# Kernel tuning notes

Measured on AMD Instinct MI355X. Metric: run time of the kernel, lower is better.

The kernel has to match this reference:

```python
import jax, jax.numpy as jnp
import numpy as np

D_MODEL = 1024
D_FF = 4096
NUM_EXPERTS = 8
TOP_K = 2


def setup_inputs() -> dict:
    key = jax.random.key(0)
    ks = jax.random.split(key, 9)
    s_in = 1.0 / np.sqrt(D_MODEL)
    s_ff = 1.0 / np.sqrt(D_FF)
    return {
        "x": jax.random.normal(ks[0], (2, 1024, D_MODEL), dtype=jnp.float32),
        "Wg": jax.random.uniform(ks[1], (D_MODEL, NUM_EXPERTS), minval=-s_in, maxval=s_in, dtype=jnp.float32),
        "bg": jax.random.uniform(ks[2], (NUM_EXPERTS,), minval=-s_in, maxval=s_in, dtype=jnp.float32),
        "W1": jax.random.uniform(ks[3], (NUM_EXPERTS, D_MODEL, D_FF), minval=-s_in, maxval=s_in, dtype=jnp.float32),
        "b1": jax.random.uniform(ks[4], (NUM_EXPERTS, D_FF), minval=-s_in, maxval=s_in, dtype=jnp.float32),
        "W2": jax.random.uniform(ks[5], (NUM_EXPERTS, D_MODEL, D_FF), minval=-s_in, maxval=s_in, dtype=jnp.float32),
        "b2": jax.random.uniform(ks[6], (NUM_EXPERTS, D_FF), minval=-s_in, maxval=s_in, dtype=jnp.float32),
        "W3": jax.random.uniform(ks[7], (NUM_EXPERTS, D_FF, D_MODEL), minval=-s_ff, maxval=s_ff, dtype=jnp.float32),
        "b3": jax.random.uniform(ks[8], (NUM_EXPERTS, D_MODEL), minval=-s_ff, maxval=s_ff, dtype=jnp.float32),
    }


def reference(x, Wg, bg, W1, b1, W2, b2, W3, b3):
    B, S, D = x.shape
    xf = x.reshape(-1, D)                                   # [N, D]
    N = xf.shape[0]

    # ---- Router (eval mode: no noise) ----
    logits = xf @ Wg + bg                                   # [N, E]
    top_logits, top_idx = jax.lax.top_k(logits, TOP_K)      # [N, K]
    top_w = jax.nn.softmax(top_logits, axis=-1)             # softmax over the top-k logits
    # scatter top-k weights into dense [N, E]; indices are unique per row
    comb_w = jnp.zeros_like(logits).at[jnp.arange(N)[:, None], top_idx].set(top_w)

    # ---- Experts: GLU-MLP, dense per-expert (weights are 0 for unrouted tokens) ----
    h1 = jnp.einsum('nd,edf->enf', xf, W1) + b1[:, None, :]  # [E, N, F]
    h2 = jnp.einsum('nd,edf->enf', xf, W2) + b2[:, None, :]
    hidden = jax.nn.gelu(h1, approximate=False) * h2         # torch nn.GELU is exact (erf)
    expert_out = jnp.einsum('enf,efd->end', hidden, W3) + b3[:, None, :]  # [E, N, D]

    # ---- Weighted combine ----
    final = jnp.einsum('end,ne->nd', expert_out, comb_w)     # [N, D]
    aux_loss = 0.0  # eval mode: aux loss inactive
    return final.reshape(B, S, D), aux_loss
```

## Files before the change

### kernel.cpp

```cpp
#include <hip/hip_runtime.h>
#include <hip/hip_bf16.h>
#include <math.h>

#define D_MODEL 1024
#define D_FF    4096
#define NE      8
#define MT      256

typedef __bf16 bf16x8 __attribute__((ext_vector_type(8)));
typedef float  f32x4  __attribute__((ext_vector_type(4)));

__device__ __forceinline__ void async16(const void* g, void* l) {
    __builtin_amdgcn_global_load_lds(
        (__attribute__((address_space(1))) uint32_t*)g,
        (__attribute__((address_space(3))) uint32_t*)l, 16, 0, 0);
}

__device__ __forceinline__ int xcd_swizzle(int lin, int nwg) {
    if ((nwg & 7) != 0) return lin;
    int q = nwg >> 3;
    return (lin & 7) * q + (lin >> 3);
}

__device__ __forceinline__ void transpose_tile_k128(
    const float* __restrict__ s, __bf16* __restrict__ d,
    int K, int N, int kt, int nt, int tid, float (*tile)[65])
{
    int tr = tid >> 4, tc = (tid & 15) * 4;
#pragma unroll
    for (int p = 0; p < 8; ++p) {
        float4 v = *reinterpret_cast<const float4*>(
            s + (size_t)(kt + tr + p * 16) * N + nt + tc);
        tile[tr + p * 16][tc + 0] = v.x;
        tile[tr + p * 16][tc + 1] = v.y;
        tile[tr + p * 16][tc + 2] = v.z;
        tile[tr + p * 16][tc + 3] = v.w;
    }
    __syncthreads();
    int kq = (tid & 15) * 8;
#pragma unroll
    for (int p = 0; p < 4; ++p) {
        int rr = (tid >> 4) + p * 16;
        bf16x8 pk;
#pragma unroll
        for (int i = 0; i < 8; ++i) pk[i] = (__bf16)tile[kq + i][rr];
        *reinterpret_cast<bf16x8*>(d + (size_t)(nt + rr) * K + kt + kq) = pk;
    }
}

__global__ __launch_bounds__(256) void fused_pre(
    const float* __restrict__ x, const float* __restrict__ Wg,
    const float* __restrict__ bg, int* __restrict__ topidx,
    float* __restrict__ topw, __bf16* __restrict__ Xb,
    const float* __restrict__ W1, const float* __restrict__ W2,
    const float* __restrict__ W3,
    __bf16* __restrict__ W1t, __bf16* __restrict__ W2t,
    __bf16* __restrict__ W3t, int nrouter)
{
    __shared__ float buf[128][65];
    int bid = blockIdx.x, tid = threadIdx.x;

    if (bid >= nrouter) {
        int tt = bid - nrouter;
        if (tt < 2 * 4096) {
            const float* s = W1; __bf16* d = W1t;
            if (tt >= 4096) { s = W2; d = W2t; tt -= 4096; }
            int e = tt >> 9, rem = tt & 511;
            int kt_i = rem >> 6, nt_i = rem & 63;
            transpose_tile_k128(s + ((size_t)e << 22), d + ((size_t)e << 22),
                                D_MODEL, D_FF, kt_i * 128, nt_i * 64, tid, buf);
        } else {
            tt -= 2 * 4096;
            int e = tt >> 9, rem = tt & 511;
            int kt_i = rem >> 4, nt_i = rem & 15;
            transpose_tile_k128(W3 + ((size_t)e << 22), W3t + ((size_t)e << 22),
                                D_FF, D_MODEL, kt_i * 128, nt_i * 64, tid, buf);
        }
        return;
    }

    int n = bid;
    const float* xr = x + (size_t)n * D_MODEL;
    int d0 = tid * 4;
    float4 xv = *reinterpret_cast<const float4*>(xr + d0);

    union { __bf16 h[4]; ushort4 u; } pk;
    pk.h[0] = (__bf16)xv.x; pk.h[1] = (__bf16)xv.y;
    pk.h[2] = (__bf16)xv.z; pk.h[3] = (__bf16)xv.w;
    *reinterpret_cast<ushort4*>(Xb + (size_t)n * D_MODEL + d0) = pk.u;

    float part[NE];
#pragma unroll
    for (int e = 0; e < NE; ++e) part[e] = 0.f;
    float xs[4] = {xv.x, xv.y, xv.z, xv.w};
#pragma unroll
    for (int j = 0; j < 4; ++j) {
        const float4* wr = reinterpret_cast<const float4*>(Wg + (size_t)(d0 + j) * NE);
        float4 w0 = wr[0], w1 = wr[1];
        part[0] += xs[j] * w0.x; part[1] += xs[j] * w0.y;
        part[2] += xs[j] * w0.z; part[3] += xs[j] * w0.w;
        part[4] += xs[j] * w1.x; part[5] += xs[j] * w1.y;
        part[6] += xs[j] * w1.z; part[7] += xs[j] * w1.w;
    }
#pragma unroll
    for (int off = 32; off > 0; off >>= 1) {
#pragma unroll
        for (int e = 0; e < NE; ++e) part[e] += __shfl_down(part[e], off);
    }
    float* sred = &buf[0][0];
    float* slog = &buf[1][0];
    int wave = tid >> 6, lane = tid & 63;
    if (lane == 0) {
#pragma unroll
        for (int e = 0; e < NE; ++e) sred[wave * NE + e] = part[e];
    }
    __syncthreads();
    if (tid < NE)
        slog[tid] = bg[tid] + sred[tid] + sred[NE + tid] + sred[2 * NE + tid] + sred[3 * NE + tid];
    __syncthreads();
    if (tid == 0) {
        float m0 = -1e30f, m1 = -1e30f; int i0 = 0, i1 = 0;
        for (int e = 0; e < NE; ++e) {
            float l = slog[e];
            if (l > m0)      { m1 = m0; i1 = i0; m0 = l; i0 = e; }
            else if (l > m1) { m1 = l;  i1 = e; }
        }
        float w1 = expf(m1 - m0);
        float s  = 1.f + w1;
        topidx[n * 2 + 0] = i0; topidx[n * 2 + 1] = i1;
        topw[n * 2 + 0] = 1.f / s; topw[n * 2 + 1] = w1 / s;
    }
}

__global__ __launch_bounds__(256) void build_lists_kernel(
    const int* __restrict__ topidx, const float* __restrict__ topw,
    int* __restrict__ pairTok, float* __restrict__ pairW,
    int* __restrict__ rbe, int* __restrict__ pairRow,
    int npairs, int maxrows, int maxblk)
{
    __shared__ int cnt[NE], cur[NE], pof[NE];
    int tid = threadIdx.x;
    if (tid < NE) { cnt[tid] = 0; cur[tid] = 0; }
    for (int i = tid; i < maxrows; i += 256) pairTok[i] = -1;
    for (int i = tid; i < maxblk; i += 256) rbe[i] = -1;
    __syncthreads();
    for (int p = tid; p < npairs; p += 256) atomicAdd(&cnt[topidx[p]], 1);
    __syncthreads();
    if (tid == 0) {
        int off = 0;
        for (int e = 0; e < NE; ++e) { pof[e] = off; off += (cnt[e] + MT - 1) & ~(MT - 1); }
        for (int e = 0; e < NE; ++e) {
            int nb = (cnt[e] + MT - 1) / MT;
            for (int j = 0; j < nb; ++j) rbe[pof[e] / MT + j] = e;
        }
    }
    __syncthreads();
    for (int p = tid; p < npairs; p += 256) {
        int e = topidx[p];
        int pos = atomicAdd(&cur[e], 1);
        int r = pof[e] + pos;
        pairTok[r]  = p >> 1;
        pairW[r]    = topw[p];
        pairRow[p]  = r;
    }
}

__global__ __launch_bounds__(512) void gemm1_mfma(
    const __bf16* __restrict__ Xb, const __bf16* __restrict__ W1t,
    const __bf16* __restrict__ W2t, const float* __restrict__ b1,
    const float* __restrict__ b2, const int* __restrict__ pairTok,
    const int* __restrict__ rbe, const __bf16* __restrict__ zpg,
    __bf16* __restrict__ hidden, int maxblk)
{
    int wgid = xcd_swizzle(blockIdx.x, gridDim.x);
    int b = wgid % maxblk;
    int e = rbe[b];
    if (e < 0) return;
    int fblk = (wgid / maxblk) * 128;

    __shared__ __bf16 smem[2][32768];

    int tid = threadIdx.x, w = tid >> 6, l = tid & 63;
    int srcslot = (l & 7) ^ (l >> 3);
    int r0 = b * MT;

    const __bf16* aptr[4];
#pragma unroll
    for (int j = 0; j < 4; ++j) {
        int row = w * 32 + j * 8 + (l >> 3);
        int tok = pairTok[r0 + row];
        aptr[j] = (tok >= 0 ? Xb + (size_t)tok * D_MODEL : zpg) + srcslot * 8;
    }
    const __bf16* b1base = W1t + ((size_t)e << 22)
        + (size_t)(fblk + w * 16 + (l >> 3)) * D_MODEL + srcslot * 8;
    const __bf16* b2base = W2t + ((size_t)e << 22)
        + (size_t)(fblk + w * 16 + (l >> 3)) * D_MODEL + srcslot * 8;

    int wm = (w >> 1) * 64, wf = (w & 1) * 64;
    int lm = l & 15;

    f32x4 c1[4][4], c2[4][4];
#pragma unroll
    for (int mi = 0; mi < 4; ++mi)
#pragma unroll
        for (int fj = 0; fj < 4; ++fj) {
            c1[mi][fj] = (f32x4){0.f, 0.f, 0.f, 0.f};
            c2[mi][fj] = (f32x4){0.f, 0.f, 0.f, 0.f};
        }

    auto stage = [&](int buf, int k0) {
        __bf16* base = &smem[buf][0];
#pragma unroll
        for (int j = 0; j < 4; ++j)
            async16(aptr[j] + k0, base + w * 2048 + j * 512);
        async16(b1base + k0,               base + 16384 + w * 1024);
        async16(b1base + 8 * D_MODEL + k0, base + 16384 + w * 1024 + 512);
        async16(b2base + k0,               base + 24576 + w * 1024);
        async16(b2base + 8 * D_MODEL + k0, base + 24576 + w * 1024 + 512);
    };

    stage(0, 0);
    __syncthreads();
    const int NT = D_MODEL / 64;
    for (int t = 0; t < NT; ++t) {
        int cur = t & 1;
        if (t + 1 < NT) stage(cur ^ 1, (t + 1) * 64);
        const __bf16* sb = &smem[cur][0];
#pragma unroll
        for (int ks = 0; ks < 2; ++ks) {
            int sl = (((ks * 4 + (l >> 4)) ^ (l & 7)) << 3);
            bf16x8 a[4];
#pragma unroll
            for (int mi = 0; mi < 4; ++mi)
                a[mi] = *reinterpret_cast<const bf16x8*>(sb + (wm + mi * 16 + lm) * 64 + sl);
#pragma unroll
            for (int fj = 0; fj < 4; ++fj) {
                int frow = wf + fj * 16 + lm;
                bf16x8 bv1 = *reinterpret_cast<const bf16x8*>(sb + 16384 + frow * 64 + sl);
                bf16x8 bv2 = *reinterpret_cast<const bf16x8*>(sb + 24576 + frow * 64 + sl);
#pragma unroll
                for (int mi = 0; mi < 4; ++mi) {
                    c1[mi][fj] = __builtin_amdgcn_mfma_f32_16x16x32_bf16(a[mi], bv1, c1[mi][fj], 0, 0, 0);
                    c2[mi][fj] = __builtin_amdgcn_mfma_f32_16x16x32_bf16(a[mi], bv2, c2[mi][fj], 0, 0, 0);
                }
            }
        }
        __syncthreads();
    }

#pragma unroll
    for (int fj = 0; fj < 4; ++fj) {
        int f = fblk + wf + fj * 16 + lm;
        float b1v = b1[e * D_FF + f];
        float b2v = b2[e * D_FF + f];
#pragma unroll
        for (int mi = 0; mi < 4; ++mi)
#pragma unroll
            for (int r = 0; r < 4; ++r) {
                int m = wm + mi * 16 + (l >> 4) * 4 + r;
                float h1 = c1[mi][fj][r] + b1v;
                float h2 = c2[mi][fj][r] + b2v;
                float g = 0.5f * h1 * (1.f + erff(h1 * 0.70710678118654752f));
                hidden[(size_t)(r0 + m) * D_FF + f] = (__bf16)(g * h2);
            }
    }
}

__global__ __launch_bounds__(512, 4) void gemm2_mfma(
    const __bf16* __restrict__ hidden, const __bf16* __restrict__ W3t,
    const float* __restrict__ b3, const int* __restrict__ rbe,
    float* __restrict__ po, int nrb)
{
    int wgid = xcd_swizzle(blockIdx.x, gridDim.x);
    int rb = wgid % nrb;
    int e = rbe[rb >> 1];
    if (e < 0) return;
    int dblk = (wgid / nrb) * 128;

    __shared__ __bf16 smem[2][16384];

    int tid = threadIdx.x, w = tid >> 6, l = tid & 63;
    int ss8 = (l & 7) ^ (l >> 3);
    int r0m = rb * 128;

    const __bf16* abase = hidden + (size_t)(r0m + w * 16 + (l >> 3)) * D_FF + ss8 * 8;
    const __bf16* bbase = W3t + ((size_t)e << 22)
        + (size_t)(dblk + w * 16 + (l >> 3)) * D_FF + ss8 * 8;

    int wm = (w >> 1) * 32, wn = (w & 1) * 64;
    int lm = l & 15;

    f32x4 c[2][4];
#pragma unroll
    for (int mi = 0; mi < 2; ++mi)
#pragma unroll
        for (int nj = 0; nj < 4; ++nj) c[mi][nj] = (f32x4){0.f, 0.f, 0.f, 0.f};

    auto stage = [&](int buf, int k0) {
        __bf16* base = &smem[buf][0];
        async16(abase + k0,              base + w * 1024 + l * 8);
        async16(abase + 8 * D_FF + k0,   base + w * 1024 + 512 + l * 8);
        async16(bbase + k0,              base + 8192 + w * 1024 + l * 8);
        async16(bbase + 8 * D_FF + k0,   base + 8192 + w * 1024 + 512 + l * 8);
    };

    stage(0, 0);
    __syncthreads();
    const int NT = D_FF / 64;
    for (int t = 0; t < NT; ++t) {
        int cur = t & 1;
        if (t + 1 < NT) stage(cur ^ 1, (t + 1) * 64);
        const __bf16* sb = &smem[cur][0];
#pragma unroll
        for (int ks = 0; ks < 2; ++ks) {
            int sl = (((ks * 4 + (l >> 4)) ^ (l & 7)) << 3);
            bf16x8 a[2];
#pragma unroll
            for (int mi = 0; mi < 2; ++mi)
                a[mi] = *reinterpret_cast<const bf16x8*>(sb + (wm + mi * 16 + lm) * 64 + sl);
#pragma unroll
            for (int nj = 0; nj < 4; ++nj) {
                bf16x8 bv = *reinterpret_cast<const bf16x8*>(sb + 8192 + (wn + nj * 16 + lm) * 64 + sl);
#pragma unroll
                for (int mi = 0; mi < 2; ++mi)
                    c[mi][nj] = __builtin_amdgcn_mfma_f32_16x16x32_bf16(a[mi], bv, c[mi][nj], 0, 0, 0);
            }
        }
        __syncthreads();
    }

#pragma unroll
    for (int nj = 0; nj < 4; ++nj) {
        int d = dblk + wn + nj * 16 + lm;
        float b3v = b3[e * D_MODEL + d];
#pragma unroll
        for (int mi = 0; mi < 2; ++mi)
#pragma unroll
            for (int r = 0; r < 4; ++r) {
                int m = wm + mi * 16 + (l >> 4) * 4 + r;
                po[(size_t)(r0m + m) * D_MODEL + d] = c[mi][nj][r] + b3v;
            }
    }
}

__global__ __launch_bounds__(256) void combine_kernel(
    const float* __restrict__ po, const float* __restrict__ topw,
    const int* __restrict__ pairRow, float* __restrict__ out)
{
    int t = blockIdx.x, tid = threadIdx.x;
    int d = tid * 4;
    float w0 = topw[t * 2], w1 = topw[t * 2 + 1];
    int r0 = pairRow[t * 2], r1 = pairRow[t * 2 + 1];
    float4 v0 = *reinterpret_cast<const float4*>(po + (size_t)r0 * D_MODEL + d);
    float4 v1 = *reinterpret_cast<const float4*>(po + (size_t)r1 * D_MODEL + d);
    float4 o;
    o.x = w0 * v0.x + w1 * v1.x;
    o.y = w0 * v0.y + w1 * v1.y;
    o.z = w0 * v0.z + w1 * v1.z;
    o.w = w0 * v0.w + w1 * v1.w;
    *reinterpret_cast<float4*>(out + (size_t)t * D_MODEL + d) = o;
}

extern "C" void kernel_launch(void* const* d_in, const int* in_sizes, int n_in,
                              void* d_out, int out_size, void* d_ws, size_t ws_size,
                              hipStream_t stream)
{
    const float* x  = (const float*)d_in[0];
    const float* Wg = (const float*)d_in[1];
    const float* bg = (const float*)d_in[2];
    const float* W1 = (const float*)d_in[3];
    const float* b1 = (const float*)d_in[4];
    const float* W2 = (const float*)d_in[5];
    const float* b2 = (const float*)d_in[6];
    const float* W3 = (const float*)d_in[7];
    const float* b3 = (const float*)d_in[8];
    float* out = (float*)d_out;

    int N = in_sizes[0] / D_MODEL;
    int npairs = N * 2;
    int maxblk = npairs / MT + NE;
    int maxrows = maxblk * MT;

    char* ws = (char*)d_ws;
    size_t off = 0;
    auto alloc = [&](size_t bytes) -> void* {
        void* p = ws + off;
        off = (off + bytes + 255) & ~(size_t)255;
        return p;
    };
    int*    topidx  = (int*)   alloc((size_t)npairs * 4);
    float*  topw    = (float*) alloc((size_t)npairs * 4);
    int*    pairTok = (int*)   alloc((size_t)maxrows * 4);
    float*  pairW   = (float*) alloc((size_t)maxrows * 4);
    int*    rbe     = (int*)   alloc((size_t)maxblk * 4);
    int*    pairRow = (int*)   alloc((size_t)npairs * 4);
    __bf16* Xb      = (__bf16*)alloc((size_t)N * D_MODEL * 2);
    __bf16* hidden  = (__bf16*)alloc((size_t)maxrows * D_FF * 2);
    __bf16* zpg     = (__bf16*)alloc(4096);
    const size_t WSZ = (size_t)NE * D_MODEL * D_FF * 2;
    __bf16* W1t = (__bf16*)alloc(WSZ);
    __bf16* W2t = (__bf16*)alloc(WSZ);
    __bf16* W3t = (__bf16*)alloc(WSZ);
    float*  po  = (float*)W1t;
    (void)ws_size; (void)n_in; (void)pairW;

    hipMemsetAsync(zpg, 0, 4096, stream);

    fused_pre<<<N + 3 * 4096, 256, 0, stream>>>(
        x, Wg, bg, topidx, topw, Xb, W1, W2, W3, W1t, W2t, W3t, N);
    build_lists_kernel<<<1, 256, 0, stream>>>(topidx, topw, pairTok, pairW, rbe,
                                              pairRow, npairs, maxrows, maxblk);
    gemm1_mfma<<<maxblk * (D_FF / 128), 512, 0, stream>>>(
        Xb, W1t, W2t, b1, b2, pairTok, rbe, zpg, hidden, maxblk);
    gemm2_mfma<<<(maxblk * 2) * (D_MODEL / 128), 512, 0, stream>>>(
        hidden, W3t, b3, rbe, po, maxblk * 2);
    combine_kernel<<<N, 256, 0, stream>>>(po, topw, pairRow, out);
}
```

Measured before the change: 332.9 us.

## Move W3 transpose-to-bf16 from preprocessing kernel into gemm1 tail

The fp32-to-bf16 transpose of W3 no longer runs in the preprocessing kernel. Each gemm1 workgroup now does a share of it after its GEMM work, two tiles per pass using the two halves of its shared memory, and idle workgroups (no expert assigned) do transpose work only. The aim is to fill gemm1's idle and tail slots with the memory-bound W3 conversion and shorten the preprocessing kernel. The risk is that transposing the full W3 (8 tiles' worth of 128x64 blocks per workgroup on average) adds to gemm1's critical path and competes with it for memory bandwidth.

After: 328.5 us. About the same (-1.3%).

```diff
diff --git a/kernel.cpp b/kernel.cpp
--- a/kernel.cpp
+++ b/kernel.cpp
@@ -6,6 +6,7 @@
 #define D_FF    4096
 #define NE      8
 #define MT      256
+#define NW3T    4096
 
 typedef __bf16 bf16x8 __attribute__((ext_vector_type(8)));
 typedef float  f32x4  __attribute__((ext_vector_type(4)));
@@ -53,29 +54,19 @@
     const float* __restrict__ bg, int* __restrict__ topidx,
     float* __restrict__ topw, __bf16* __restrict__ Xb,
     const float* __restrict__ W1, const float* __restrict__ W2,
-    const float* __restrict__ W3,
-    __bf16* __restrict__ W1t, __bf16* __restrict__ W2t,
-    __bf16* __restrict__ W3t, int nrouter)
+    __bf16* __restrict__ W1t, __bf16* __restrict__ W2t, int nrouter)
 {
     __shared__ float buf[128][65];
     int bid = blockIdx.x, tid = threadIdx.x;
 
     if (bid >= nrouter) {
         int tt = bid - nrouter;
-        if (tt < 2 * 4096) {
-            const float* s = W1; __bf16* d = W1t;
-            if (tt >= 4096) { s = W2; d = W2t; tt -= 4096; }
-            int e = tt >> 9, rem = tt & 511;
-            int kt_i = rem >> 6, nt_i = rem & 63;
-            transpose_tile_k128(s + ((size_t)e << 22), d + ((size_t)e << 22),
-                                D_MODEL, D_FF, kt_i * 128, nt_i * 64, tid, buf);
-        } else {
-            tt -= 2 * 4096;
-            int e = tt >> 9, rem = tt & 511;
-            int kt_i = rem >> 4, nt_i = rem & 15;
-            transpose_tile_k128(W3 + ((size_t)e << 22), W3t + ((size_t)e << 22),
-                                D_FF, D_MODEL, kt_i * 128, nt_i * 64, tid, buf);
-        }
+        const float* s = W1; __bf16* d = W1t;
+        if (tt >= 4096) { s = W2; d = W2t; tt -= 4096; }
+        int e = tt >> 9, rem = tt & 511;
+        int kt_i = rem >> 6, nt_i = rem & 63;
+        transpose_tile_k128(s + ((size_t)e << 22), d + ((size_t)e << 22),
+                            D_MODEL, D_FF, kt_i * 128, nt_i * 64, tid, buf);
         return;
     }
 
@@ -170,99 +161,119 @@
     const __bf16* __restrict__ W2t, const float* __restrict__ b1,
     const float* __restrict__ b2, const int* __restrict__ pairTok,
     const int* __restrict__ rbe, const __bf16* __restrict__ zpg,
-    __bf16* __restrict__ hidden, int maxblk)
-{
+    __bf16* __restrict__ hidden,
+    const float* __restrict__ W3, __bf16* __restrict__ W3t, int maxblk)
+{
+    __shared__ __bf16 smem[2][32768];
     int wgid = xcd_swizzle(blockIdx.x, gridDim.x);
     int b = wgid % maxblk;
     int e = rbe[b];
-    if (e < 0) return;
     int fblk = (wgid / maxblk) * 128;
-
-    __shared__ __bf16 smem[2][32768];
-
     int tid = threadIdx.x, w = tid >> 6, l = tid & 63;
-    int srcslot = (l & 7) ^ (l >> 3);
-    int r0 = b * MT;
-
-    const __bf16* aptr[4];
-#pragma unroll
-    for (int j = 0; j < 4; ++j) {
-        int row = w * 32 + j * 8 + (l >> 3);
-        int tok = pairTok[r0 + row];
-        aptr[j] = (tok >= 0 ? Xb + (size_t)tok * D_MODEL : zpg) + srcslot * 8;
-    }
-    const __bf16* b1base = W1t + ((size_t)e << 22)
-        + (size_t)(fblk + w * 16 + (l >> 3)) * D_MODEL + srcslot * 8;
-    const __bf16* b2base = W2t + ((size_t)e << 22)
-        + (size_t)(fblk + w * 16 + (l >> 3)) * D_MODEL + srcslot * 8;
-
-    int wm = (w >> 1) * 64, wf = (w & 1) * 64;
-    int lm = l & 15;
-
-    f32x4 c1[4][4], c2[4][4];
-#pragma unroll
-    for (int mi = 0; mi < 4; ++mi)
-#pragma unroll
-        for (int fj = 0; fj < 4; ++fj) {
-            c1[mi][fj] = (f32x4){0.f, 0.f, 0.f, 0.f};
-            c2[mi][fj] = (f32x4){0.f, 0.f, 0.f, 0.f};
-        }
-
-    auto stage = [&](int buf, int k0) {
-        __bf16* base = &smem[buf][0];
-#pragma unroll
-        for (int j = 0; j < 4; ++j)
-            async16(aptr[j] + k0, base + w * 2048 + j * 512);
-        async16(b1base + k0,               base + 16384 + w * 1024);
-        async16(b1base + 8 * D_MODEL + k0, base + 16384 + w * 1024 + 512);
-        async16(b2base + k0,               base + 24576 + w * 1024);
-        async16(b2base + 8 * D_MODEL + k0, base + 24576 + w * 1024 + 512);
-    };
-
-    stage(0, 0);
-    __syncthreads();
-    const int NT = D_MODEL / 64;
-    for (int t = 0; t < NT; ++t) {
-        int cur = t & 1;
-        if (t + 1 < NT) stage(cur ^ 1, (t + 1) * 64);
-        const __bf16* sb = &smem[cur][0];
-#pragma unroll
-        for (int ks = 0; ks < 2; ++ks) {
-            int sl = (((ks * 4 + (l >> 4)) ^ (l & 7)) << 3);
-            bf16x8 a[4];
-#pragma unroll
-            for (int mi = 0; mi < 4; ++mi)
-                a[mi] = *reinterpret_cast<const bf16x8*>(sb + (wm + mi * 16 + lm) * 64 + sl);
+
+    if (e >= 0) {
+        int srcslot = (l & 7) ^ (l >> 3);
+        int r0 = b * MT;
+
+        const __bf16* aptr[4];
+#pragma unroll
+        for (int j = 0; j < 4; ++j) {
+            int row = w * 32 + j * 8 + (l >> 3);
+            int tok = pairTok[r0 + row];
+            aptr[j] = (tok >= 0 ? Xb + (size_t)tok * D_MODEL : zpg) + srcslot * 8;
+        }
+        const __bf16* b1base = W1t + ((size_t)e << 22)
+            + (size_t)(fblk + w * 16 + (l >> 3)) * D_MODEL + srcslot * 8;
+        const __bf16* b2base = W2t + ((size_t)e << 22)
+            + (size_t)(fblk + w * 16 + (l >> 3)) * D_MODEL + srcslot * 8;
+
+        int wm = (w >> 1) * 64, wf = (w & 1) * 64;
+        int lm = l & 15;
+
+        f32x4 c1[4][4], c2[4][4];
+#pragma unroll
+        for (int mi = 0; mi < 4; ++mi)
 #pragma unroll
             for (int fj = 0; fj < 4; ++fj) {
-                int frow = wf + fj * 16 + lm;
-                bf16x8 bv1 = *reinterpret_cast<const bf16x8*>(sb + 16384 + frow * 64 + sl);
-                bf16x8 bv2 = *reinterpret_cast<const bf16x8*>(sb + 24576 + frow * 64 + sl);
-#pragma unroll
-                for (int mi = 0; mi < 4; ++mi) {
-                    c1[mi][fj] = __builtin_amdgcn_mfma_f32_16x16x32_bf16(a[mi], bv1, c1[mi][fj], 0, 0, 0);
-                    c2[mi][fj] = __builtin_amdgcn_mfma_f32_16x16x32_bf16(a[mi], bv2, c2[mi][fj], 0, 0, 0);
+                c1[mi][fj] = (f32x4){0.f, 0.f, 0.f, 0.f};
+                c2[mi][fj] = (f32x4){0.f, 0.f, 0.f, 0.f};
+            }
+
+        auto stage = [&](int buf, int k0) {
+            __bf16* base = &smem[buf][0];
+#pragma unroll
+            for (int j = 0; j < 4; ++j)
+                async16(aptr[j] + k0, base + w * 2048 + j * 512);
+            async16(b1base + k0,               base + 16384 + w * 1024);
+            async16(b1base + 8 * D_MODEL + k0, base + 16384 + w * 1024 + 512);
+            async16(b2base + k0,               base + 24576 + w * 1024);
+            async16(b2base + 8 * D_MODEL + k0, base + 24576 + w * 1024 + 512);
+        };
+
+        stage(0, 0);
+        __syncthreads();
+        const int NT = D_MODEL / 64;
+        for (int t = 0; t < NT; ++t) {
+            int cur = t & 1;
+            if (t + 1 < NT) stage(cur ^ 1, (t + 1) * 64);
+            const __bf16* sb = &smem[cur][0];
+#pragma unroll
+            for (int ks = 0; ks < 2; ++ks) {
+                int sl = (((ks * 4 + (l >> 4)) ^ (l & 7)) << 3);
+                bf16x8 a[4];
+#pragma unroll
+                for (int mi = 0; mi < 4; ++mi)
+                    a[mi] = *reinterpret_cast<const bf16x8*>(sb + (wm + mi * 16 + lm) * 64 + sl);
+#pragma unroll
+                for (int fj = 0; fj < 4; ++fj) {
+                    int frow = wf + fj * 16 + lm;
+                    bf16x8 bv1 = *reinterpret_cast<const bf16x8*>(sb + 16384 + frow * 64 + sl);
+                    bf16x8 bv2 = *reinterpret_cast<const bf16x8*>(sb + 24576 + frow * 64 + sl);
+#pragma unroll
+                    for (int mi = 0; mi < 4; ++mi) {
+                        c1[mi][fj] = __builtin_amdgcn_mfma_f32_16x16x32_bf16(a[mi], bv1, c1[mi][fj], 0, 0, 0);
+                        c2[mi][fj] = __builtin_amdgcn_mfma_f32_16x16x32_bf16(a[mi], bv2, c2[mi][fj], 0, 0, 0);
+                    }
                 }
             }
+            __syncthreads();
+        }
+
+#pragma unroll
+        for (int fj = 0; fj < 4; ++fj) {
+            int f = fblk + wf + fj * 16 + lm;
+            float b1v = b1[e * D_FF + f];
+            float b2v = b2[e * D_FF + f];
+#pragma unroll
+            for (int mi = 0; mi < 4; ++mi)
+#pragma unroll
+                for (int r = 0; r < 4; ++r) {
+                    int m = wm + mi * 16 + (l >> 4) * 4 + r;
+                    float h1 = c1[mi][fj][r] + b1v;
+                    float h2 = c2[mi][fj][r] + b2v;
+                    float g = 0.5f * h1 * (1.f + erff(h1 * 0.70710678118654752f));
+                    hidden[(size_t)(r0 + m) * D_FF + f] = (__bf16)(g * h2);
+                }
         }
         __syncthreads();
     }
 
-#pragma unroll
-    for (int fj = 0; fj < 4; ++fj) {
-        int f = fblk + wf + fj * 16 + lm;
-        float b1v = b1[e * D_FF + f];
-        float b2v = b2[e * D_FF + f];
-#pragma unroll
-        for (int mi = 0; mi < 4; ++mi)
-#pragma unroll
-            for (int r = 0; r < 4; ++r) {
-                int m = wm + mi * 16 + (l >> 4) * 4 + r;
-                float h1 = c1[mi][fj][r] + b1v;
-                float h2 = c2[mi][fj][r] + b2v;
-                float g = 0.5f * h1 * (1.f + erff(h1 * 0.70710678118654752f));
-                hidden[(size_t)(r0 + m) * D_FF + f] = (__bf16)(g * h2);
-            }
+    {
+        int nwg = gridDim.x;
+        float* smf = reinterpret_cast<float*>(&smem[0][0]);
+        int sub = tid >> 8;
+        float (*tb)[65] = reinterpret_cast<float (*)[65]>(smf + sub * 8520);
+        int stid = tid & 255;
+        for (int t0 = wgid; t0 < NW3T; t0 += 2 * nwg) {
+            int t1 = t0 + nwg;
+            if (t1 >= NW3T) t1 = t0;
+            int tt = sub ? t1 : t0;
+            int te = tt >> 9, rem = tt & 511;
+            int kt_i = rem >> 4, nt_i = rem & 15;
+            transpose_tile_k128(W3 + ((size_t)te << 22), W3t + ((size_t)te << 22),
+                                D_FF, D_MODEL, kt_i * 128, nt_i * 64, stid, tb);
+            __syncthreads();
+        }
     }
 }
 
@@ -406,12 +417,12 @@
 
     hipMemsetAsync(zpg, 0, 4096, stream);
 
-    fused_pre<<<N + 3 * 4096, 256, 0, stream>>>(
-        x, Wg, bg, topidx, topw, Xb, W1, W2, W3, W1t, W2t, W3t, N);
+    fused_pre<<<N + 2 * 4096, 256, 0, stream>>>(
+        x, Wg, bg, topidx, topw, Xb, W1, W2, W1t, W2t, N);
     build_lists_kernel<<<1, 256, 0, stream>>>(topidx, topw, pairTok, pairW, rbe,
                                               pairRow, npairs, maxrows, maxblk);
     gemm1_mfma<<<maxblk * (D_FF / 128), 512, 0, stream>>>(
-        Xb, W1t, W2t, b1, b2, pairTok, rbe, zpg, hidden, maxblk);
+        Xb, W1t, W2t, b1, b2, pairTok, rbe, zpg, hidden, W3, W3t, maxblk);
     gemm2_mfma<<<(maxblk * 2) * (D_MODEL / 128), 512, 0, stream>>>(
         hidden, W3t, b3, rbe, po, maxblk * 2);
     combine_kernel<<<N, 256, 0, stream>>>(po, topw, pairRow, out);
```
